# Kernel tuning notes

Hardware: AMD Instinct MI355X
Metric: run time of the kernel (lower is better)

Reference implementation:

```python
import jax, jax.numpy as jnp
import numpy as np

D_MODEL = 2048
NUM_HEADS = 16
D_KV = D_MODEL // NUM_HEADS
THETA = 10000.0


def apply_rope(x, pos):
    # x: [B, H, S, d_kv], pos: [S] int
    d = x.shape[-1]
    inv_freq = 1.0 / (THETA ** (jnp.arange(0, d, 2, dtype=jnp.float32) / d))  # [d/2]
    ang = pos.astype(jnp.float32)[:, None] * inv_freq[None, :]  # [S, d/2]
    cos, sin = jnp.cos(ang), jnp.sin(ang)  # broadcast over B,H
    x1 = x[..., 0::2]
    x2 = x[..., 1::2]
    r1 = x1 * cos - x2 * sin
    r2 = x1 * sin + x2 * cos
    return jnp.stack([r1, r2], axis=-1).reshape(x.shape)


def setup_inputs() -> dict:
    key = jax.random.key(0)
    k = jax.random.split(key, 5)
    B, S = 2, 2048
    x = jax.random.normal(k[0], (B, S, D_MODEL), dtype=jnp.float32)
    scale = 1.0 / np.sqrt(D_MODEL)
    Wq = jax.random.normal(k[1], (D_MODEL, D_MODEL), dtype=jnp.float32) * scale
    Wk = jax.random.normal(k[2], (D_MODEL, D_MODEL), dtype=jnp.float32) * scale
    Wv = jax.random.normal(k[3], (D_MODEL, D_MODEL), dtype=jnp.float32) * scale
    Wo = jax.random.normal(k[4], (D_MODEL, D_MODEL), dtype=jnp.float32) * scale
    token_position = jnp.arange(S, dtype=jnp.int64 if jax.config.jax_enable_x64 else jnp.int32)
    return {"x": x, "Wq": Wq, "Wk": Wk, "Wv": Wv, "Wo": Wo, "token_position": token_position}


def reference(x, Wq, Wk, Wv, Wo, token_position):
    B, S, _ = x.shape
    def heads(y):
        return y.reshape(B, S, NUM_HEADS, D_KV).transpose(0, 2, 1, 3)  # [B,H,S,d]
    Q = heads(jnp.einsum('bsd,df->bsf', x, Wq))
    K = heads(jnp.einsum('bsd,df->bsf', x, Wk))
    V = heads(jnp.einsum('bsd,df->bsf', x, Wv))
    Q = apply_rope(Q, token_position)
    K = apply_rope(K, token_position)
    scale = 1.0 / jnp.sqrt(jnp.asarray(D_KV, dtype=x.dtype))
    scores = jnp.einsum('bhqd,bhkd->bhqk', Q, K) * scale  # [B,H,S,S]
    causal = jnp.tril(jnp.ones((S, S), dtype=bool))
    scores = jnp.where(causal, scores, -jnp.inf)
    attn = jax.nn.softmax(scores, axis=-1)
    out = jnp.einsum('bhqk,bhkd->bhqd', attn, V)  # [B,H,S,d]
    out = out.transpose(0, 2, 1, 3).reshape(B, S, D_MODEL)
    return jnp.einsum('bsd,df->bsf', out, Wo)
```

## Files before the change

kernel.cpp:

```cpp
#include <hip/hip_runtime.h>
#include <hip/hip_bf16.h>

#define S 2048
#define DM 2048
#define NH 16
#define DH 128

typedef __attribute__((ext_vector_type(8))) short short8;
typedef __attribute__((ext_vector_type(4))) float floatx4;
typedef unsigned short u16;
typedef unsigned int u32;

__device__ __forceinline__ u16 f2bf(float f) {
  union { float f; u32 u; } v; v.f = f;
  u32 r = v.u + 0x7fffu + ((v.u >> 16) & 1u);
  return (u16)(r >> 16);
}
__device__ __forceinline__ u32 pack2(float lo, float hi) {
  float2 f; f.x = lo; f.y = hi;
  __hip_bfloat162 h = __float22bfloat162_rn(f);
  union { __hip_bfloat162 h; u32 u; } c; c.h = h;
  return c.u;
}

__device__ __forceinline__ floatx4 mfma16(short8 a, short8 b, floatx4 c) {
  return __builtin_amdgcn_mfma_f32_16x16x32_bf16(a, b, c, 0, 0, 0);
}

__device__ __forceinline__ void async_cp16(const u16* g, u16* l) {
  __builtin_amdgcn_global_load_lds(
      (const __attribute__((address_space(1))) void*)g,
      (__attribute__((address_space(3))) void*)l, 16, 0, 0);
}

__global__ void conv_x_k(const float* __restrict__ x, u16* __restrict__ xb) {
  int gid = blockIdx.x * 256 + threadIdx.x;
  float4 v = ((const float4*)x)[gid];
  uint2 p; p.x = pack2(v.x, v.y); p.y = pack2(v.z, v.w);
  ((uint2*)xb)[gid] = p;
}

__global__ void conv_w_k(const float* __restrict__ W0, const float* __restrict__ W1,
                         const float* __restrict__ W2, const float* __restrict__ W3,
                         u16* __restrict__ out) {
  __shared__ float tile[32][33];
  const float* W = blockIdx.z == 0 ? W0 : blockIdx.z == 1 ? W1 : blockIdx.z == 2 ? W2 : W3;
  u16* O = out + (size_t)blockIdx.z * DM * DM;
  int tx = threadIdx.x & 31, ty = threadIdx.x >> 5;
  int k0 = blockIdx.y * 32, n0 = blockIdx.x * 32;
#pragma unroll
  for (int j = 0; j < 4; j++)
    tile[ty + j * 8][tx] = W[(size_t)(k0 + ty + j * 8) * DM + n0 + tx];
  __syncthreads();
#pragma unroll
  for (int j = 0; j < 4; j++)
    O[(size_t)(n0 + ty + j * 8) * DM + k0 + tx] = f2bf(tile[tx][ty + j * 8]);
}

#define BM 256
#define BN 256
#define BK 64

#define BARRIER __builtin_amdgcn_s_barrier()
#define SB __builtin_amdgcn_sched_barrier(0)
#define LGKM0 asm volatile("s_waitcnt lgkmcnt(0)" ::: "memory")

#define STG_A(q, j, koff) \
  async_cp16(pAg + (size_t)(j) * 64 * DM + (koff), &As[q][soff + (j) * 4096])
#define STG_B(q, j, koff) \
  async_cp16(pBg + (size_t)(j) * 64 * DM + (koff), &Bs[q][soff + (j) * 4096])

#define PH0(p, q, koff, PRE) { \
    a0k0 = *(const short8*)&As[p][awb + xk0]; \
    a0k1 = *(const short8*)&As[p][awb + xk1]; \
    a1k0 = *(const short8*)&As[p][awb + 1024 + xk0]; \
    a1k1 = *(const short8*)&As[p][awb + 1024 + xk1]; \
    a2k0 = *(const short8*)&As[p][awb + 2048 + xk0]; \
    a2k1 = *(const short8*)&As[p][awb + 2048 + xk1]; \
    a3k0 = *(const short8*)&As[p][awb + 3072 + xk0]; \
    a3k1 = *(const short8*)&As[p][awb + 3072 + xk1]; \
    b0k0 = *(const short8*)&Bs[p][bwb + xk0]; \
    b0k1 = *(const short8*)&Bs[p][bwb + xk1]; \
    b1k0 = *(const short8*)&Bs[p][bwb + 1024 + xk0]; \
    b1k1 = *(const short8*)&Bs[p][bwb + 1024 + xk1]; \
    if (PRE) { STG_A(q, 0, koff); STG_A(q, 1, koff); \
               STG_A(q, 2, koff); STG_A(q, 3, koff); } \
    BARRIER; LGKM0; SB; \
    __builtin_amdgcn_s_setprio(1); \
    acc[0][0] = mfma16(a0k0, b0k0, acc[0][0]); \
    acc[1][0] = mfma16(a1k0, b0k0, acc[1][0]); \
    acc[2][0] = mfma16(a2k0, b0k0, acc[2][0]); \
    acc[3][0] = mfma16(a3k0, b0k0, acc[3][0]); \
    acc[0][1] = mfma16(a0k0, b1k0, acc[0][1]); \
    acc[1][1] = mfma16(a1k0, b1k0, acc[1][1]); \
    acc[2][1] = mfma16(a2k0, b1k0, acc[2][1]); \
    acc[3][1] = mfma16(a3k0, b1k0, acc[3][1]); \
    acc[0][0] = mfma16(a0k1, b0k1, acc[0][0]); \
    acc[1][0] = mfma16(a1k1, b0k1, acc[1][0]); \
    acc[2][0] = mfma16(a2k1, b0k1, acc[2][0]); \
    acc[3][0] = mfma16(a3k1, b0k1, acc[3][0]); \
    acc[0][1] = mfma16(a0k1, b1k1, acc[0][1]); \
    acc[1][1] = mfma16(a1k1, b1k1, acc[1][1]); \
    acc[2][1] = mfma16(a2k1, b1k1, acc[2][1]); \
    acc[3][1] = mfma16(a3k1, b1k1, acc[3][1]); \
    __builtin_amdgcn_s_setprio(0); \
    BARRIER; }

#define PH1(p, q, koff, PRE) { \
    b2k0 = *(const short8*)&Bs[p][bwb + 2048 + xk0]; \
    b2k1 = *(const short8*)&Bs[p][bwb + 2048 + xk1]; \
    b3k0 = *(const short8*)&Bs[p][bwb + 3072 + xk0]; \
    b3k1 = *(const short8*)&Bs[p][bwb + 3072 + xk1]; \
    if (PRE) { STG_B(q, 0, koff); STG_B(q, 1, koff); \
               STG_B(q, 2, koff); STG_B(q, 3, koff); } \
    BARRIER; LGKM0; SB; \
    __builtin_amdgcn_s_setprio(1); \
    acc[0][2] = mfma16(a0k0, b2k0, acc[0][2]); \
    acc[1][2] = mfma16(a1k0, b2k0, acc[1][2]); \
    acc[2][2] = mfma16(a2k0, b2k0, acc[2][2]); \
    acc[3][2] = mfma16(a3k0, b2k0, acc[3][2]); \
    acc[0][3] = mfma16(a0k0, b3k0, acc[0][3]); \
    acc[1][3] = mfma16(a1k0, b3k0, acc[1][3]); \
    acc[2][3] = mfma16(a2k0, b3k0, acc[2][3]); \
    acc[3][3] = mfma16(a3k0, b3k0, acc[3][3]); \
    acc[0][2] = mfma16(a0k1, b2k1, acc[0][2]); \
    acc[1][2] = mfma16(a1k1, b2k1, acc[1][2]); \
    acc[2][2] = mfma16(a2k1, b2k1, acc[2][2]); \
    acc[3][2] = mfma16(a3k1, b2k1, acc[3][2]); \
    acc[0][3] = mfma16(a0k1, b3k1, acc[0][3]); \
    acc[1][3] = mfma16(a1k1, b3k1, acc[1][3]); \
    acc[2][3] = mfma16(a2k1, b3k1, acc[2][3]); \
    acc[3][3] = mfma16(a3k1, b3k1, acc[3][3]); \
    __builtin_amdgcn_s_setprio(0); \
    BARRIER; }

#define PH2(p) { \
    a0k0 = *(const short8*)&As[p][awb + 4096 + xk0]; \
    a0k1 = *(const short8*)&As[p][awb + 4096 + xk1]; \
    a1k0 = *(const short8*)&As[p][awb + 5120 + xk0]; \
    a1k1 = *(const short8*)&As[p][awb + 5120 + xk1]; \
    a2k0 = *(const short8*)&As[p][awb + 6144 + xk0]; \
    a2k1 = *(const short8*)&As[p][awb + 6144 + xk1]; \
    a3k0 = *(const short8*)&As[p][awb + 7168 + xk0]; \
    a3k1 = *(const short8*)&As[p][awb + 7168 + xk1]; \
    BARRIER; LGKM0; SB; \
    __builtin_amdgcn_s_setprio(1); \
    acc[4][0] = mfma16(a0k0, b0k0, acc[4][0]); \
    acc[5][0] = mfma16(a1k0, b0k0, acc[5][0]); \
    acc[6][0] = mfma16(a2k0, b0k0, acc[6][0]); \
    acc[7][0] = mfma16(a3k0, b0k0, acc[7][0]); \
    acc[4][1] = mfma16(a0k0, b1k0, acc[4][1]); \
    acc[5][1] = mfma16(a1k0, b1k0, acc[5][1]); \
    acc[6][1] = mfma16(a2k0, b1k0, acc[6][1]); \
    acc[7][1] = mfma16(a3k0, b1k0, acc[7][1]); \
    acc[4][0] = mfma16(a0k1, b0k1, acc[4][0]); \
    acc[5][0] = mfma16(a1k1, b0k1, acc[5][0]); \
    acc[6][0] = mfma16(a2k1, b0k1, acc[6][0]); \
    acc[7][0] = mfma16(a3k1, b0k1, acc[7][0]); \
    acc[4][1] = mfma16(a0k1, b1k1, acc[4][1]); \
    acc[5][1] = mfma16(a1k1, b1k1, acc[5][1]); \
    acc[6][1] = mfma16(a2k1, b1k1, acc[6][1]); \
    acc[7][1] = mfma16(a3k1, b1k1, acc[7][1]); \
    __builtin_amdgcn_s_setprio(0); \
    BARRIER; }

#define PH3(PRE) { \
    __builtin_amdgcn_s_setprio(1); \
    acc[4][2] = mfma16(a0k0, b2k0, acc[4][2]); \
    acc[5][2] = mfma16(a1k0, b2k0, acc[5][2]); \
    acc[6][2] = mfma16(a2k0, b2k0, acc[6][2]); \
    acc[7][2] = mfma16(a3k0, b2k0, acc[7][2]); \
    acc[4][3] = mfma16(a0k0, b3k0, acc[4][3]); \
    acc[5][3] = mfma16(a1k0, b3k0, acc[5][3]); \
    acc[6][3] = mfma16(a2k0, b3k0, acc[6][3]); \
    acc[7][3] = mfma16(a3k0, b3k0, acc[7][3]); \
    acc[4][2] = mfma16(a0k1, b2k1, acc[4][2]); \
    acc[5][2] = mfma16(a1k1, b2k1, acc[5][2]); \
    acc[6][2] = mfma16(a2k1, b2k1, acc[6][2]); \
    acc[7][2] = mfma16(a3k1, b2k1, acc[7][2]); \
    acc[4][3] = mfma16(a0k1, b3k1, acc[4][3]); \
    acc[5][3] = mfma16(a1k1, b3k1, acc[5][3]); \
    acc[6][3] = mfma16(a2k1, b3k1, acc[6][3]); \
    acc[7][3] = mfma16(a3k1, b3k1, acc[7][3]); \
    __builtin_amdgcn_s_setprio(0); SB; \
    if (PRE) { asm volatile("s_waitcnt vmcnt(0)" ::: "memory"); BARRIER; SB; } }

#define TILE(p, q, koff, PRE) \
    PH0(p, q, koff, PRE) PH1(p, q, koff, PRE) PH2(p) PH3(PRE)

__global__ __launch_bounds__(512, 2)
void gemm_k(const u16* __restrict__ A, const u16* __restrict__ Wt,
            u16* __restrict__ oQ, u16* __restrict__ oK, u16* __restrict__ oV,
            float* __restrict__ oO, const int* __restrict__ tp, int opmode)
{
  __shared__ u16 As[2][BM * BK];
  __shared__ u16 Bs[2][BN * BK];
  const int t = threadIdx.x;
  const int w = t >> 6, lane = t & 63;
  const int l16 = lane & 15, quad = lane >> 4;
  const int wr = w >> 2, wc = w & 3;
  const int m0 = blockIdx.y * BM, n0 = blockIdx.x * BN;
  const u16* Bt = Wt + (size_t)(opmode == 1 ? 3 : blockIdx.z) * DM * DM;

  const int srow = t >> 3;
  const int sc = ((t & 7) ^ (srow & 7)) * 8;
  const u16* pAg = A + (size_t)(m0 + srow) * DM + sc;
  const u16* pBg = Bt + (size_t)(n0 + srow) * DM + sc;
  const int soff = t * 8;

  const int awb = (wr * 128 + l16) * 64;
  const int bwb = (wc * 64 + l16) * 64;
  const int xk0 = ((quad) ^ (l16 & 7)) << 3;
  const int xk1 = ((4 + quad) ^ (l16 & 7)) << 3;

  floatx4 acc[8][4] = {};
  short8 a0k0, a0k1, a1k0, a1k1, a2k0, a2k1, a3k0, a3k1;
  short8 b0k0, b0k1, b1k0, b1k1, b2k0, b2k1, b3k0, b3k1;

#pragma unroll
  for (int j = 0; j < 4; j++) STG_A(0, j, 0);
#pragma unroll
  for (int j = 0; j < 4; j++) STG_B(0, j, 0);
  SB;
  asm volatile("s_waitcnt vmcnt(0)" ::: "memory");
  BARRIER; SB;

  for (int it = 0; it < 16; ++it) {
    const int kA = (2 * it + 1) * 64;
    const int kB = (2 * it + 2) * 64;
    TILE(0, 1, kA, 1)
    TILE(1, 0, kB, it < 15)
  }

  const int mode = (opmode == 1) ? 3 : ((int)blockIdx.z == 2 ? 2 : 0);
  const int mwb = m0 + wr * 128;
  const int nwb = n0 + wc * 64;
  if (mode == 3) {
#pragma unroll
    for (int mi = 0; mi < 8; mi++) {
      int m = mwb + mi * 16 + quad * 4;
#pragma unroll
      for (int ni = 0; ni < 4; ni++) {
        int n = nwb + ni * 16 + l16;
#pragma unroll
        for (int r = 0; r < 4; r++)
          oO[(size_t)(m + r) * DM + n] = acc[mi][ni][r];
      }
    }
  } else if (mode == 2) {
#pragma unroll
    for (int mi = 0; mi < 8; mi++) {
      int m = mwb + mi * 16 + quad * 4;
      int b = m >> 11, s = m & (S - 1);
#pragma unroll
      for (int ni = 0; ni < 4; ni++) {
        int f = nwb + ni * 16 + l16;
        int h = f >> 7, dh = f & (DH - 1);
        uint2 pk; pk.x = pack2(acc[mi][ni][0], acc[mi][ni][1]);
        pk.y = pack2(acc[mi][ni][2], acc[mi][ni][3]);
        *(uint2*)&oV[((size_t)(b * NH + h) * DH + dh) * S + s] = pk;
      }
    }
  } else {
    u16* Out = ((int)blockIdx.z == 0) ? oQ : oK;
    const float qs = ((int)blockIdx.z == 0) ? 0.12752780f : 1.0f;
#pragma unroll
    for (int mi = 0; mi < 8; mi++) {
#pragma unroll
      for (int r = 0; r < 4; r++) {
        int m = mwb + mi * 16 + quad * 4 + r;
        int b = m >> 11, s = m & (S - 1);
        int ps = tp[s];
#pragma unroll
        for (int ni = 0; ni < 4; ni++) {
          int f = nwb + ni * 16 + l16;
          int h = f >> 7, dh = f & (DH - 1);
          float own = acc[mi][ni][r];
          float oth = __shfl_xor(own, 1, 64);
          float fr = __expf((float)(dh & ~1) * (-9.210340371976184f / 128.0f));
          float ang = (float)ps * fr;
          float sn, cs; __sincosf(ang, &sn, &cs);
          float res = (dh & 1) ? (oth * sn + own * cs) : (own * cs - oth * sn);
          Out[((size_t)(b * NH + h) * S + s) * DH + dh] = f2bf(res * qs);
        }
      }
    }
  }
}

__global__ __launch_bounds__(256, 4)
void attn_k(const u16* __restrict__ Q, const u16* __restrict__ K,
            const u16* __restrict__ Vt, u16* __restrict__ O)
{
  __shared__ u16 Ks[64 * 128];
  __shared__ u16 Vs[128 * 64];
  __shared__ u16 P[4][16 * 64];
  const int t = threadIdx.x, w = t >> 6, lane = t & 63;
  const int l16 = lane & 15, quad = lane >> 4;
  const int task = blockIdx.x;
  const int bh = task & 31, b = bh >> 4, h = bh & 15;
  const int g = 31 - (task >> 5);
  const int qg = g * 64;
  const int qt = qg + w * 16;
  const u16* Qb = Q + (size_t)bh * S * DH;
  const u16* Kb = K + (size_t)bh * S * DH;
  const u16* Vb = Vt + (size_t)bh * DH * S;
  u16* Pw = P[w];
  const int pxor = l16 & 7;

  const u16* pK[4]; u16* lK[4];
  const u16* pV[4]; u16* lV[4];
#pragma unroll
  for (int j = 0; j < 4; j++) {
    int kr = w * 16 + j * 4 + (lane >> 4);
    int ks = lane & 15;
    int kc = ks ^ (kr & 15);
    pK[j] = Kb + (size_t)kr * DH + kc * 8;
    lK[j] = &Ks[kr * 128 + ks * 8];
    int vr = w * 32 + j * 8 + (lane >> 3);
    int vs = lane & 7;
    int vc = vs ^ (vr & 7);
    pV[j] = Vb + (size_t)vr * S + vc * 8;
    lV[j] = &Vs[vr * 64 + vs * 8];
  }

  short8 aq[4];
#pragma unroll
  for (int kc = 0; kc < 4; kc++)
    aq[kc] = *(const short8*)&Qb[(size_t)(qt + l16) * DH + kc * 32 + quad * 8];

  floatx4 o[8] = {};
  float lsum = 0.0f;
  const int kend = qg + 64;

  for (int k0 = 0; k0 < kend; k0 += 64) {
#pragma unroll
    for (int j = 0; j < 4; j++) async_cp16(pK[j] + (size_t)k0 * DH, lK[j]);
#pragma unroll
    for (int j = 0; j < 4; j++) async_cp16(pV[j] + k0, lV[j]);
    __syncthreads();

    floatx4 sc[4] = {};
#pragma unroll
    for (int hh = 0; hh < 4; hh++) {
      int row = hh * 16 + l16;
#pragma unroll
      for (int kc = 0; kc < 4; kc++) {
        short8 kf = *(short8*)&Ks[row * 128 + (((kc * 4 + quad) ^ l16) << 3)];
        sc[hh] = mfma16(kf, aq[kc], sc[hh]);
      }
    }
    if (k0 + 64 > qt) {
#pragma unroll
      for (int hh = 0; hh < 4; hh++)
#pragma unroll
        for (int r = 0; r < 4; r++) {
          int j = k0 + hh * 16 + quad * 4 + r;
          if (j > qt + l16) sc[hh][r] = -3.0e38f;
        }
    }
#pragma unroll
    for (int hh = 0; hh < 4; hh++) {
      float e0 = __builtin_amdgcn_exp2f(fminf(sc[hh][0], 44.0f));
      float e1 = __builtin_amdgcn_exp2f(fminf(sc[hh][1], 44.0f));
      float e2 = __builtin_amdgcn_exp2f(fminf(sc[hh][2], 44.0f));
      float e3 = __builtin_amdgcn_exp2f(fminf(sc[hh][3], 44.0f));
      lsum += (e0 + e1) + (e2 + e3);
      uint2 pk; pk.x = pack2(e0, e1); pk.y = pack2(e2, e3);
      int su = (2 * hh + (quad >> 1)) ^ pxor;
      *(uint2*)&Pw[l16 * 64 + su * 8 + (quad & 1) * 4] = pk;
    }
    asm volatile("s_waitcnt lgkmcnt(0)" ::: "memory");
#pragma unroll
    for (int c = 0; c < 2; c++) {
      short8 pf = *(short8*)&Pw[l16 * 64 + (((4 * c + quad) ^ pxor) << 3)];
#pragma unroll
      for (int t8 = 0; t8 < 8; t8++) {
        int row = t8 * 16 + l16;
        short8 av = *(short8*)&Vs[row * 64 + (((c * 4 + quad) ^ (l16 & 7)) << 3)];
        o[t8] = mfma16(av, pf, o[t8]);
      }
    }
    __syncthreads();
  }

  float l = lsum + __shfl_xor(lsum, 16, 64);
  l += __shfl_xor(l, 32, 64);
  float inv = __builtin_amdgcn_rcpf(l);
#pragma unroll
  for (int t8 = 0; t8 < 8; t8++) {
    uint2 pa;
    pa.x = pack2(o[t8][0] * inv, o[t8][1] * inv);
    pa.y = pack2(o[t8][2] * inv, o[t8][3] * inv);
    *(uint2*)&O[((size_t)(b * S + qt + l16)) * DM + h * DH + t8 * 16 + quad * 4] = pa;
  }
}

extern "C" void kernel_launch(void* const* d_in, const int* in_sizes, int n_in,
                              void* d_out, int out_size, void* d_ws, size_t ws_size,
                              hipStream_t stream) {
  const float* x  = (const float*)d_in[0];
  const float* Wq = (const float*)d_in[1];
  const float* Wk = (const float*)d_in[2];
  const float* Wv = (const float*)d_in[3];
  const float* Wo = (const float*)d_in[4];
  const int*   tp = (const int*)d_in[5];

  char* ws = (char*)d_ws;
  u16* Wt = (u16*)ws;
  u16* xb = (u16*)(ws + 33554432);
  u16* Qb = (u16*)(ws + 50331648);
  u16* Kb = (u16*)(ws + 67108864);
  u16* Vb = (u16*)(ws + 83886080);
  u16* Ob = (u16*)(ws + 100663296);

  conv_x_k<<<8192, 256, 0, stream>>>(x, xb);
  conv_w_k<<<dim3(64, 64, 4), 256, 0, stream>>>(Wq, Wk, Wv, Wo, Wt);
  gemm_k<<<dim3(8, 16, 3), 512, 0, stream>>>(xb, Wt, Qb, Kb, Vb, nullptr, tp, 0);
  attn_k<<<1024, 256, 0, stream>>>(Qb, Kb, Vb, Ob);
  gemm_k<<<dim3(8, 16, 1), 512, 0, stream>>>(Ob, Wt, nullptr, nullptr,
                                             nullptr, (float*)d_out, tp, 1);
}
```

Before: 388.2 us.

## Use dedicated smaller-tile kernel for output projection and add MFMA priority hints in attention

Moves the output projection off the 256x256-tile QKV GEMM, which ran only 128 blocks on a 256-CU part, into a new 128x128-tile kernel with 512 blocks. The new kernel uses a simple single-buffered, K=32 async-copy loop. The attention kernel also raises wave priority around its two MFMA sections with s_setprio. The aim is better CU occupancy for the output GEMM, at the cost of less software pipelining and more barriers per K step.

After: 378.3 us. 1.03x faster.

```diff
diff --git a/kernel.cpp b/kernel.cpp
--- a/kernel.cpp
+++ b/kernel.cpp
@@ -191,7 +191,7 @@
 __global__ __launch_bounds__(512, 2)
 void gemm_k(const u16* __restrict__ A, const u16* __restrict__ Wt,
             u16* __restrict__ oQ, u16* __restrict__ oK, u16* __restrict__ oV,
-            float* __restrict__ oO, const int* __restrict__ tp, int opmode)
+            const int* __restrict__ tp)
 {
   __shared__ u16 As[2][BM * BK];
   __shared__ u16 Bs[2][BN * BK];
@@ -200,7 +200,7 @@
   const int l16 = lane & 15, quad = lane >> 4;
   const int wr = w >> 2, wc = w & 3;
   const int m0 = blockIdx.y * BM, n0 = blockIdx.x * BN;
-  const u16* Bt = Wt + (size_t)(opmode == 1 ? 3 : blockIdx.z) * DM * DM;
+  const u16* Bt = Wt + (size_t)blockIdx.z * DM * DM;
 
   const int srow = t >> 3;
   const int sc = ((t & 7) ^ (srow & 7)) * 8;
@@ -232,22 +232,9 @@
     TILE(1, 0, kB, it < 15)
   }
 
-  const int mode = (opmode == 1) ? 3 : ((int)blockIdx.z == 2 ? 2 : 0);
   const int mwb = m0 + wr * 128;
   const int nwb = n0 + wc * 64;
-  if (mode == 3) {
-#pragma unroll
-    for (int mi = 0; mi < 8; mi++) {
-      int m = mwb + mi * 16 + quad * 4;
-#pragma unroll
-      for (int ni = 0; ni < 4; ni++) {
-        int n = nwb + ni * 16 + l16;
-#pragma unroll
-        for (int r = 0; r < 4; r++)
-          oO[(size_t)(m + r) * DM + n] = acc[mi][ni][r];
-      }
-    }
-  } else if (mode == 2) {
+  if ((int)blockIdx.z == 2) {
 #pragma unroll
     for (int mi = 0; mi < 8; mi++) {
       int m = mwb + mi * 16 + quad * 4;
@@ -284,6 +271,72 @@
           Out[((size_t)(b * NH + h) * S + s) * DH + dh] = f2bf(res * qs);
         }
       }
+    }
+  }
+}
+
+__global__ __launch_bounds__(256, 4)
+void oproj_k(const u16* __restrict__ A, const u16* __restrict__ Wt,
+             float* __restrict__ oO)
+{
+  __shared__ u16 As2[128 * 32];
+  __shared__ u16 Bs2[128 * 32];
+  const int t = threadIdx.x;
+  const int w = t >> 6, lane = t & 63;
+  const int l16 = lane & 15, quad = lane >> 4;
+  const int m0 = blockIdx.y * 128, n0 = blockIdx.x * 128;
+  const int wm = (w >> 1) * 64, wn = (w & 1) * 64;
+  const u16* Bt = Wt + (size_t)3 * DM * DM;
+
+  const u16* pA[2]; const u16* pB[2]; u16* lA[2]; u16* lB[2];
+#pragma unroll
+  for (int i = 0; i < 2; i++) {
+    int unit = i * 256 + t;
+    int row = unit >> 2, s = unit & 3;
+    int c = s ^ ((row >> 1) & 3);
+    pA[i] = A + (size_t)(m0 + row) * DM + c * 8;
+    pB[i] = Bt + (size_t)(n0 + row) * DM + c * 8;
+    lA[i] = &As2[unit * 8];
+    lB[i] = &Bs2[unit * 8];
+  }
+
+  floatx4 acc[4][4] = {};
+
+  for (int k0 = 0; k0 < DM; k0 += 32) {
+#pragma unroll
+    for (int i = 0; i < 2; i++) {
+      async_cp16(pA[i] + k0, lA[i]);
+      async_cp16(pB[i] + k0, lB[i]);
+    }
+    __syncthreads();
+    short8 af[4], bfr[4];
+#pragma unroll
+    for (int i = 0; i < 4; i++) {
+      int row = wm + i * 16 + l16;
+      af[i] = *(short8*)&As2[(row * 4 + (quad ^ ((row >> 1) & 3))) * 8];
+    }
+#pragma unroll
+    for (int i = 0; i < 4; i++) {
+      int row = wn + i * 16 + l16;
+      bfr[i] = *(short8*)&Bs2[(row * 4 + (quad ^ ((row >> 1) & 3))) * 8];
+    }
+#pragma unroll
+    for (int mi = 0; mi < 4; mi++)
+#pragma unroll
+      for (int ni = 0; ni < 4; ni++)
+        acc[mi][ni] = mfma16(af[mi], bfr[ni], acc[mi][ni]);
+    __syncthreads();
+  }
+
+#pragma unroll
+  for (int mi = 0; mi < 4; mi++) {
+    int m = m0 + wm + mi * 16 + quad * 4;
+#pragma unroll
+    for (int ni = 0; ni < 4; ni++) {
+      int n = n0 + wn + ni * 16 + l16;
+#pragma unroll
+      for (int r = 0; r < 4; r++)
+        oO[(size_t)(m + r) * DM + n] = acc[mi][ni][r];
     }
   }
 }
@@ -341,6 +394,7 @@
     __syncthreads();
 
     floatx4 sc[4] = {};
+    __builtin_amdgcn_s_setprio(1);
 #pragma unroll
     for (int hh = 0; hh < 4; hh++) {
       int row = hh * 16 + l16;
@@ -350,6 +404,7 @@
         sc[hh] = mfma16(kf, aq[kc], sc[hh]);
       }
     }
+    __builtin_amdgcn_s_setprio(0);
     if (k0 + 64 > qt) {
 #pragma unroll
       for (int hh = 0; hh < 4; hh++)
@@ -371,6 +426,7 @@
       *(uint2*)&Pw[l16 * 64 + su * 8 + (quad & 1) * 4] = pk;
     }
     asm volatile("s_waitcnt lgkmcnt(0)" ::: "memory");
+    __builtin_amdgcn_s_setprio(1);
 #pragma unroll
     for (int c = 0; c < 2; c++) {
       short8 pf = *(short8*)&Pw[l16 * 64 + (((4 * c + quad) ^ pxor) << 3)];
@@ -381,6 +437,7 @@
         o[t8] = mfma16(av, pf, o[t8]);
       }
     }
+    __builtin_amdgcn_s_setprio(0);
     __syncthreads();
   }
 
@@ -416,8 +473,7 @@
 
   conv_x_k<<<8192, 256, 0, stream>>>(x, xb);
   conv_w_k<<<dim3(64, 64, 4), 256, 0, stream>>>(Wq, Wk, Wv, Wo, Wt);
-  gemm_k<<<dim3(8, 16, 3), 512, 0, stream>>>(xb, Wt, Qb, Kb, Vb, nullptr, tp, 0);
+  gemm_k<<<dim3(8, 16, 3), 512, 0, stream>>>(xb, Wt, Qb, Kb, Vb, tp);
   attn_k<<<1024, 256, 0, stream>>>(Qb, Kb, Vb, Ob);
-  gemm_k<<<dim3(8, 16, 1), 512, 0, stream>>>(Ob, Wt, nullptr, nullptr,
-                                             nullptr, (float*)d_out, tp, 1);
-}
+  oproj_k<<<dim3(16, 32), 256, 0, stream>>>(Ob, Wt, (float*)d_out);
+}
```
